# Kernel tuning notes

Measured on AMD Instinct MI355X. Metric: run time of the kernel, lower is better.

The kernel has to match this reference:

```python
import jax, jax.numpy as jnp
import numpy as np


def setup_inputs() -> dict:
    key = jax.random.key(0)
    kA, kB = jax.random.split(key)
    B_, m, n, d = 32, 1024, 1024, 128
    A = jax.random.normal(kA, (B_, m, d), dtype=jnp.float32)
    B = jax.random.normal(kB, (B_, n, d), dtype=jnp.float32)
    return {"A": A, "B": B}


def reference(A, B):
    # e[b,i,j] = <A[b,i], B[b,j]>  -- unnormalized alignment scores
    e = jnp.einsum("bmd,bnd->bmn", A, B)
    # beta[b,i] = sum_j softmax_j(e[b,i,:]) * B[b,j]  (hypothesis aligned to premise)
    beta = jnp.einsum("bmn,bnd->bmd", jax.nn.softmax(e, axis=-1), B)
    # alpha[b,j] = sum_i softmax_i(e[b,:,j]) * A[b,i]  (premise aligned to hypothesis)
    alpha = jnp.einsum("bmn,bmd->bnd", jax.nn.softmax(e, axis=1), A)
    return beta, alpha
```

## Files before the change

### kernel.cpp

```cpp
#include <hip/hip_runtime.h>
#include <hip/hip_bf16.h>
#include <stdint.h>

typedef __attribute__((ext_vector_type(4))) float f32x4;
typedef __attribute__((ext_vector_type(8))) _Float16 f16x8;
typedef __attribute__((ext_vector_type(2))) __fp16 fp16x2;

#define NB 32
#define MM 1024
#define DD 128
#define BKV 64
#define NTILE (MM / BKV)
#define LOG2E 1.44269504089f
#define RTHR 6.0f

static constexpr size_t ARR = (size_t)NB * MM * DD;


__device__ __forceinline__ float fexp2(float x) { return __builtin_amdgcn_exp2f(x); }

__device__ __forceinline__ void gl16(const void* g, void* l) {
  __builtin_amdgcn_global_load_lds((const __attribute__((address_space(1))) void*)g,
                                   (__attribute__((address_space(3))) void*)l, 16, 0, 0);
}

__global__ __launch_bounds__(256) void prep_kernel(const float* __restrict__ A,
                                                   const float* __restrict__ B,
                                                   _Float16* __restrict__ ws) {
  const int rt = blockIdx.x;
  const int b  = blockIdx.y;
  const int wh = blockIdx.z;
  const float* __restrict__ src = wh ? B : A;
  _Float16* __restrict__ Xh  = ws + (size_t)wh * ARR;
  _Float16* __restrict__ XTh = ws + 2 * ARR + (size_t)wh * ARR;

  __shared__ __align__(16) _Float16 tile[64][130];
  const int t = threadIdx.x;

#pragma unroll
  for (int it = 0; it < 4; ++it) {
    int id  = it * 256 + t;
    int row = id >> 4;
    int ch  = id & 15;
    int grow = rt * 64 + row;
    const float* p = src + ((size_t)(b * MM + grow) * DD + ch * 8);
    float4 x0 = *(const float4*)p;
    float4 x1 = *(const float4*)(p + 4);
    f16x8 h;
    h[0] = (_Float16)x0.x; h[1] = (_Float16)x0.y; h[2] = (_Float16)x0.z; h[3] = (_Float16)x0.w;
    h[4] = (_Float16)x1.x; h[5] = (_Float16)x1.y; h[6] = (_Float16)x1.z; h[7] = (_Float16)x1.w;
    char* dst = (char*)Xh + (((size_t)(b * MM + grow)) << 8) + ((ch << 4) ^ ((row & 7) << 4));
    *(f16x8*)dst = h;
#pragma unroll
    for (int j = 0; j < 8; ++j) tile[row][ch * 8 + j] = h[j];
  }
  __syncthreads();

#pragma unroll
  for (int it = 0; it < 4; ++it) {
    int id = it * 256 + t;
    int d  = id >> 3;
    int ch = id & 7;
    f16x8 h;
#pragma unroll
    for (int j = 0; j < 8; ++j) {
      int i = ch * 8 + j;
      int s = (i & 0x23) | ((i & 4) << 2) | ((i & 24) >> 1);
      h[j] = tile[s][d];
    }
    char* dst = (char*)XTh + (((size_t)(b * DD + d)) << 11) + (rt << 7)
              + ((ch << 4) ^ ((d & 7) << 4));
    *(f16x8*)dst = h;
  }
}

__global__ __launch_bounds__(256, 2) void attn_kernel(const _Float16* __restrict__ ws,
                                                      float* __restrict__ out) {
  const int g   = blockIdx.x;
  const int x   = g & 7;
  const int t2  = g >> 3;
  const int qt  = t2 & 7;
  const int p   = ((t2 >> 3) << 3) | x;
  const int b   = p & 31;
  const int dir = p >> 5;

  const _Float16* __restrict__ Qh  = ws + (dir ? ARR : 0);
  const _Float16* __restrict__ Kh  = ws + (dir ? 0 : ARR);
  const _Float16* __restrict__ VTh = ws + 2 * ARR + (dir ? 0 : ARR);
  float* __restrict__ outp = out + (size_t)dir * ARR;

  __shared__ __align__(16) char sbuf[2][32768];

  const int tid  = threadIdx.x;
  const int w    = tid >> 6;
  const int lane = tid & 63;
  const int lrow = lane & 15;
  const int lgrp = lane >> 4;

  const int q0 = qt * 128 + w * 32 + lrow;

  f16x8 qf[2][4];
  {
    const int swz = (lrow & 7) << 4;
#pragma unroll
    for (int qb = 0; qb < 2; ++qb) {
      const char* qbase = (const char*)Qh + (((size_t)(b * MM + q0 + qb * 16)) << 8);
#pragma unroll
      for (int kc = 0; kc < 4; ++kc)
        qf[qb][kc] = *(const f16x8*)(qbase + ((kc * 64 + lgrp * 16) ^ swz));
    }
  }

  const int pl  = (lgrp * 16) ^ ((lrow & 3) << 4);
  const int lb6 = (lrow & 4) << 4;
  const int kE = lrow * 256 + pl + lb6;
  const int kO = lrow * 256 + pl + (64 - lb6);
  const int vE = 16384 + lrow * 128 + pl + lb6;
  const int vO = 16384 + lrow * 128 + pl + (64 - lb6);

  const char* ksrc = (const char*)Kh + (((size_t)b * MM) << 8) + (size_t)tid * 16;
  const char* vsrc = (const char*)VTh + (((size_t)b * DD) << 11)
                   + ((size_t)(tid >> 3) << 11) + (size_t)(tid & 7) * 16;

  f32x4 oacc[2][8];
#pragma unroll
  for (int qb = 0; qb < 2; ++qb)
#pragma unroll
    for (int dt = 0; dt < 8; ++dt) oacc[qb][dt] = (f32x4)0.0f;
  float mrun[2] = {-1e30f, -1e30f};
  float lrun[2] = {0.0f, 0.0f};

  f16x8 vreg[16];
  f16x8 pf[2][2];

  {
    char* sb = sbuf[0];
#pragma unroll
    for (int it = 0; it < 4; ++it)
      gl16(ksrc + it * 4096, sb + it * 4096 + tid * 16);
#pragma unroll
    for (int it = 0; it < 4; ++it)
      gl16(vsrc + it * 65536, sb + 16384 + it * 4096 + tid * 16);
  }
  asm volatile("s_waitcnt vmcnt(0)" ::: "memory");
  __syncthreads();

#pragma unroll 1
  for (int t = 0; t < NTILE; ++t) {
    const char* base = sbuf[t & 1];

    if (t + 1 < NTILE) {
      char* sb = sbuf[(t + 1) & 1];
      const char* kp = ksrc + (size_t)(t + 1) * 16384;
      const char* vp = vsrc + (size_t)(t + 1) * 128;
#pragma unroll
      for (int it = 0; it < 4; ++it)
        gl16(kp + it * 4096, sb + it * 4096 + tid * 16);
#pragma unroll
      for (int it = 0; it < 4; ++it)
        gl16(vp + it * 65536, sb + 16384 + it * 4096 + tid * 16);
    }

    f32x4 sc[2][4];
#pragma unroll
    for (int qb = 0; qb < 2; ++qb)
#pragma unroll
      for (int nt = 0; nt < 4; ++nt) sc[qb][nt] = (f32x4)0.0f;
#pragma unroll
    for (int nt = 0; nt < 4; ++nt) {
#pragma unroll
      for (int kc = 0; kc < 4; ++kc) {
        const int off = ((kc & 1) ? kO + (kc - 1) * 64 : kE + kc * 64) + nt * 4096;
        f16x8 kf = *(const f16x8*)(base + off);
        sc[0][nt] = __builtin_amdgcn_mfma_f32_16x16x32_f16(kf, qf[0][kc], sc[0][nt], 0, 0, 0);
        sc[1][nt] = __builtin_amdgcn_mfma_f32_16x16x32_f16(kf, qf[1][kc], sc[1][nt], 0, 0, 0);
      }
    }

    if (t > 0) {
#pragma unroll
      for (int dt = 0; dt < 8; ++dt) {
        oacc[0][dt] = __builtin_amdgcn_mfma_f32_16x16x32_f16(vreg[dt * 2 + 0], pf[0][0], oacc[0][dt], 0, 0, 0);
        oacc[0][dt] = __builtin_amdgcn_mfma_f32_16x16x32_f16(vreg[dt * 2 + 1], pf[0][1], oacc[0][dt], 0, 0, 0);
        oacc[1][dt] = __builtin_amdgcn_mfma_f32_16x16x32_f16(vreg[dt * 2 + 0], pf[1][0], oacc[1][dt], 0, 0, 0);
        oacc[1][dt] = __builtin_amdgcn_mfma_f32_16x16x32_f16(vreg[dt * 2 + 1], pf[1][1], oacc[1][dt], 0, 0, 0);
      }
    }

    float mx[2];
#pragma unroll
    for (int qb = 0; qb < 2; ++qb) {
      float a0 = fmaxf(fmaxf(sc[qb][0][0], sc[qb][0][1]), fmaxf(sc[qb][0][2], sc[qb][0][3]));
      float a1 = fmaxf(fmaxf(sc[qb][1][0], sc[qb][1][1]), fmaxf(sc[qb][1][2], sc[qb][1][3]));
      float a2 = fmaxf(fmaxf(sc[qb][2][0], sc[qb][2][1]), fmaxf(sc[qb][2][2], sc[qb][2][3]));
      float a3 = fmaxf(fmaxf(sc[qb][3][0], sc[qb][3][1]), fmaxf(sc[qb][3][2], sc[qb][3][3]));
      mx[qb] = fmaxf(fmaxf(a0, a1), fmaxf(a2, a3));
    }
    bool need = (mx[0] > mrun[0] + RTHR) || (mx[1] > mrun[1] + RTHR);
    if (__any(need)) {
#pragma unroll
      for (int qb = 0; qb < 2; ++qb) {
        float cm = mx[qb];
        cm = fmaxf(cm, __shfl_xor(cm, 16));
        cm = fmaxf(cm, __shfl_xor(cm, 32));
        float mnew = fmaxf(mrun[qb], cm);
        float scale = fexp2((mrun[qb] - mnew) * LOG2E);
        lrun[qb] *= scale;
#pragma unroll
        for (int dt = 0; dt < 8; ++dt) oacc[qb][dt] *= scale;
        mrun[qb] = mnew;
      }
    }

#pragma unroll
    for (int qb = 0; qb < 2; ++qb) {
      union { fp16x2 h[8]; f16x8 v[2]; } u;
      float ps = 0.0f;
      const float nml = -mrun[qb] * LOG2E;
#pragma unroll
      for (int nt = 0; nt < 4; ++nt) {
        float p0 = fexp2(fmaf(sc[qb][nt][0], LOG2E, nml));
        float p1 = fexp2(fmaf(sc[qb][nt][1], LOG2E, nml));
        float p2 = fexp2(fmaf(sc[qb][nt][2], LOG2E, nml));
        float p3 = fexp2(fmaf(sc[qb][nt][3], LOG2E, nml));
        ps += (p0 + p1) + (p2 + p3);
        u.h[nt * 2 + 0] = __builtin_amdgcn_cvt_pkrtz(p0, p1);
        u.h[nt * 2 + 1] = __builtin_amdgcn_cvt_pkrtz(p2, p3);
      }
      lrun[qb] += ps;
      pf[qb][0] = u.v[0];
      pf[qb][1] = u.v[1];
    }

#pragma unroll
    for (int dt = 0; dt < 8; ++dt) {
      vreg[dt * 2 + 0] = *(const f16x8*)(base + vE + dt * 2048);
      vreg[dt * 2 + 1] = *(const f16x8*)(base + vO + dt * 2048);
    }

    asm volatile("s_waitcnt vmcnt(0)" ::: "memory");
    __syncthreads();
  }

#pragma unroll
  for (int dt = 0; dt < 8; ++dt) {
    oacc[0][dt] = __builtin_amdgcn_mfma_f32_16x16x32_f16(vreg[dt * 2 + 0], pf[0][0], oacc[0][dt], 0, 0, 0);
    oacc[0][dt] = __builtin_amdgcn_mfma_f32_16x16x32_f16(vreg[dt * 2 + 1], pf[0][1], oacc[0][dt], 0, 0, 0);
    oacc[1][dt] = __builtin_amdgcn_mfma_f32_16x16x32_f16(vreg[dt * 2 + 0], pf[1][0], oacc[1][dt], 0, 0, 0);
    oacc[1][dt] = __builtin_amdgcn_mfma_f32_16x16x32_f16(vreg[dt * 2 + 1], pf[1][1], oacc[1][dt], 0, 0, 0);
  }

#pragma unroll
  for (int qb = 0; qb < 2; ++qb) {
    float l = lrun[qb];
    l += __shfl_xor(l, 16);
    l += __shfl_xor(l, 32);
    float inv = __builtin_amdgcn_rcpf(l);
    float* op = outp + ((size_t)(b * MM + q0 + qb * 16)) * DD + lgrp * 4;
#pragma unroll
    for (int dt = 0; dt < 8; ++dt) {
      f32x4 v = oacc[qb][dt] * inv;
      *(f32x4*)(op + dt * 16) = v;
    }
  }
}

extern "C" void kernel_launch(void* const* d_in, const int* in_sizes, int n_in,
                              void* d_out, int out_size, void* d_ws, size_t ws_size,
                              hipStream_t stream) {
  const float* A = (const float*)d_in[0];
  const float* B = (const float*)d_in[1];
  float* out = (float*)d_out;
  if (ws_size < 4 * ARR * sizeof(_Float16)) return;
  _Float16* ws = (_Float16*)d_ws;

  dim3 blk(256, 1, 1);
  dim3 g1(16, 32, 2);
  prep_kernel<<<g1, blk, 0, stream>>>(A, B, ws);
  dim3 g2(512, 1, 1);
  attn_kernel<<<g2, blk, 0, stream>>>(ws, out);
}
```

Measured before the change: 58.60 us.

## Load V tiles directly from global into registers instead of staging through LDS

Removes V from the LDS double buffer, halving shared memory. Each wave now loads its V fragments straight from global memory into registers, overlapped with the score computation. The per-iteration wait becomes a partial vmcnt, so only the K prefetch is waited on before the barrier and the V loads stay in flight. This cuts LDS traffic and barrier pressure. In exchange, each block's four waves all read the same V data from global memory/L2 with strided per-lane accesses, and those register loads may stall the next MFMA.

After: 64.83 us. 1.11x slower.

```diff
diff --git a/kernel.cpp b/kernel.cpp
--- a/kernel.cpp
+++ b/kernel.cpp
@@ -89,7 +89,7 @@
   const _Float16* __restrict__ VTh = ws + 2 * ARR + (dir ? 0 : ARR);
   float* __restrict__ outp = out + (size_t)dir * ARR;
 
-  __shared__ __align__(16) char sbuf[2][32768];
+  __shared__ __align__(16) char sbuf[2][16384];
 
   const int tid  = threadIdx.x;
   const int w    = tid >> 6;
@@ -115,12 +115,13 @@
   const int lb6 = (lrow & 4) << 4;
   const int kE = lrow * 256 + pl + lb6;
   const int kO = lrow * 256 + pl + (64 - lb6);
-  const int vE = 16384 + lrow * 128 + pl + lb6;
-  const int vO = 16384 + lrow * 128 + pl + (64 - lb6);
+
+  const char* vgE = (const char*)VTh + (((size_t)(b * DD)) << 11)
+                  + (size_t)lrow * 2048 + (pl + lb6);
+  const char* vgO = (const char*)VTh + (((size_t)(b * DD)) << 11)
+                  + (size_t)lrow * 2048 + (pl + (64 - lb6));
 
   const char* ksrc = (const char*)Kh + (((size_t)b * MM) << 8) + (size_t)tid * 16;
-  const char* vsrc = (const char*)VTh + (((size_t)b * DD) << 11)
-                   + ((size_t)(tid >> 3) << 11) + (size_t)(tid & 7) * 16;
 
   f32x4 oacc[2][8];
 #pragma unroll
@@ -133,17 +134,12 @@
   f16x8 vreg[16];
   f16x8 pf[2][2];
 
-  {
-    char* sb = sbuf[0];
-#pragma unroll
-    for (int it = 0; it < 4; ++it)
-      gl16(ksrc + it * 4096, sb + it * 4096 + tid * 16);
-#pragma unroll
-    for (int it = 0; it < 4; ++it)
-      gl16(vsrc + it * 65536, sb + 16384 + it * 4096 + tid * 16);
-  }
+#pragma unroll
+  for (int it = 0; it < 4; ++it)
+    gl16(ksrc + it * 4096, sbuf[0] + it * 4096 + tid * 16);
   asm volatile("s_waitcnt vmcnt(0)" ::: "memory");
-  __syncthreads();
+  __builtin_amdgcn_s_barrier();
+  __builtin_amdgcn_sched_barrier(0);
 
 #pragma unroll 1
   for (int t = 0; t < NTILE; ++t) {
@@ -152,13 +148,9 @@
     if (t + 1 < NTILE) {
       char* sb = sbuf[(t + 1) & 1];
       const char* kp = ksrc + (size_t)(t + 1) * 16384;
-      const char* vp = vsrc + (size_t)(t + 1) * 128;
 #pragma unroll
       for (int it = 0; it < 4; ++it)
         gl16(kp + it * 4096, sb + it * 4096 + tid * 16);
-#pragma unroll
-      for (int it = 0; it < 4; ++it)
-        gl16(vp + it * 65536, sb + 16384 + it * 4096 + tid * 16);
     }
 
     f32x4 sc[2][4];
@@ -184,6 +176,16 @@
         oacc[0][dt] = __builtin_amdgcn_mfma_f32_16x16x32_f16(vreg[dt * 2 + 1], pf[0][1], oacc[0][dt], 0, 0, 0);
         oacc[1][dt] = __builtin_amdgcn_mfma_f32_16x16x32_f16(vreg[dt * 2 + 0], pf[1][0], oacc[1][dt], 0, 0, 0);
         oacc[1][dt] = __builtin_amdgcn_mfma_f32_16x16x32_f16(vreg[dt * 2 + 1], pf[1][1], oacc[1][dt], 0, 0, 0);
+      }
+    }
+
+    {
+      const char* ve = vgE + (size_t)t * 128;
+      const char* vo = vgO + (size_t)t * 128;
+#pragma unroll
+      for (int dt = 0; dt < 8; ++dt) {
+        vreg[dt * 2 + 0] = *(const f16x8*)(ve + (size_t)dt * 32768);
+        vreg[dt * 2 + 1] = *(const f16x8*)(vo + (size_t)dt * 32768);
       }
     }
 
@@ -232,14 +234,10 @@
       pf[qb][1] = u.v[1];
     }
 
-#pragma unroll
-    for (int dt = 0; dt < 8; ++dt) {
-      vreg[dt * 2 + 0] = *(const f16x8*)(base + vE + dt * 2048);
-      vreg[dt * 2 + 1] = *(const f16x8*)(base + vO + dt * 2048);
-    }
-
-    asm volatile("s_waitcnt vmcnt(0)" ::: "memory");
-    __syncthreads();
+    __builtin_amdgcn_sched_barrier(0);
+    asm volatile("s_waitcnt vmcnt(16)" ::: "memory");
+    __builtin_amdgcn_s_barrier();
+    __builtin_amdgcn_sched_barrier(0);
   }
 
 #pragma unroll
```
